# Performance work log

Measured on AMD Instinct MI355X. Metric: run time of the kernel, lower is better.

## Reference

```python
import jax, jax.numpy as jnp
import numpy as np

EPS = 1e-7  # keras.backend.epsilon()
B, U, F = 1024, 256, 31
D = 1 + U + F  # features dim after concat


def setup_inputs() -> dict:
    key = jax.random.key(0)
    ks = jax.random.split(key, 9)
    s = 1.0 / np.sqrt(D)
    return {
        "last_cell": jax.random.uniform(ks[0], (B, U), dtype=jnp.float32),
        "input_precipitation": jax.random.uniform(ks[1], (B,), dtype=jnp.float32),
        "input_other_features": jax.random.normal(ks[2], (B, F), dtype=jnp.float32),
        "W_i": jax.random.normal(ks[3], (D, U), dtype=jnp.float32) * s,
        "b_i": jnp.zeros((U,), dtype=jnp.float32),
        "W_r": jax.random.normal(ks[4], (D, U * U), dtype=jnp.float32) * s,
        "b_r": jnp.zeros((U * U,), dtype=jnp.float32),
        "W_o": jax.random.normal(ks[5], (D, U), dtype=jnp.float32) * s,
        "b_o": jnp.zeros((U,), dtype=jnp.float32),
    }


def reference(last_cell, input_precipitation, input_other_features,
              W_i, b_i, W_r, b_r, W_o, b_o):
    # L1-normalize last cell state (mass fractions)
    l1 = jnp.sum(jnp.abs(last_cell), axis=-1, keepdims=True) + EPS
    last_cell_hat = last_cell / l1
    p = input_precipitation[:, None]  # [B,1]
    features = jnp.concatenate([p, last_cell_hat, input_other_features], axis=-1)  # [B,D]

    # input gate: sigmoid then L1-normalized across units (mass-conserving split)
    ig = jax.nn.sigmoid(features @ W_i + b_i)
    ig = ig / jnp.sum(jnp.abs(ig), axis=-1, keepdims=True)

    # redistribution matrix: relu, reshape [B,U,U], L1-normalize each row
    R = jax.nn.relu(features @ W_r + b_r).reshape(-1, U, U)
    R = R / jnp.sum(jnp.abs(R), axis=-1, keepdims=True)

    # output gate: sigmoid
    og = jax.nn.sigmoid(features @ W_o + b_o)

    cell_in = ig * p                                   # [B,U]
    cell_sys = jnp.einsum('bu,buv->bv', last_cell, R)  # batched (1xU)@(UxU)
    candidate = cell_in + cell_sys
    output = og * candidate
    cell = (1.0 - og) * candidate
    return (cell, output)
```

## Files before the change

### kernel.cpp

```cpp
#include <hip/hip_runtime.h>


#define EPS_L1 1e-7f

constexpr int BB  = 1024;
constexpr int U   = 256;
constexpr int F   = 31;
constexpr int D   = 1 + U + F;
constexpr int NBV = BB * U;
constexpr int NCH = D / 32;
constexpr int UIMGB = NCH * 16384;
constexpr size_t WTB_BYTES  = (size_t)258 * UIMGB;
constexpr size_t FEAT_BYTES = (size_t)BB * D * 2;
constexpr int PITCH = 260;

typedef float f32x4 __attribute__((ext_vector_type(4)));
typedef short bf16x8 __attribute__((ext_vector_type(8)));

__device__ __forceinline__ unsigned f2bf(float x) {
  union { float f; unsigned u; } v; v.f = x;
  unsigned r = v.u + 0x7FFFu + ((v.u >> 16) & 1u);
  return r >> 16;
}

#define GLDS16(gp, lp)                                                        \
  __builtin_amdgcn_global_load_lds(                                          \
      (const __attribute__((address_space(1))) void*)(gp),                   \
      (__attribute__((address_space(3))) void*)(lp), 16, 0, 0)

#define MFMA16(a, b, c) __builtin_amdgcn_mfma_f32_16x16x32_bf16((a), (b), (c), 0, 0, 0)

__global__ __launch_bounds__(256) void k_prep(
    const float* __restrict__ lc, const float* __restrict__ p,
    const float* __restrict__ other,
    const float* __restrict__ Wi, const float* __restrict__ Wr,
    const float* __restrict__ Wo,
    short* __restrict__ WtB, short* __restrict__ featImg,
    float* __restrict__ cell_sys) {
  __shared__ short lds[2][32 * PITCH];
  __shared__ float inv_s[64];
  const int bid = blockIdx.x, t = threadIdx.x;

  if (bid < 774) {
    const int u = bid / 3, part = bid % 3;
    const float* src; long ld;
    if (u < 256)       { src = Wr + (size_t)u * 256; ld = 65536; }
    else if (u == 256) { src = Wi; ld = 256; }
    else               { src = Wo; ld = 256; }
    short* dst = WtB + (size_t)u * 73728;
    const int lane = t & 63, wave = t >> 6;
    const int g = lane >> 4, l15 = lane & 15;

#pragma unroll
    for (int cc = 0; cc < 3; ++cc) {
      const int c = part * 3 + cc;
      short* buf = lds[cc & 1];
#pragma unroll
      for (int i = 0; i < 8; ++i) {
        const int f = i * 256 + t;
        const int row = f >> 6, col4 = f & 63;
        const float4 v = *(const float4*)(src + (size_t)(c * 32 + row) * ld + col4 * 4);
        const unsigned lo = f2bf(v.x) | (f2bf(v.y) << 16);
        const unsigned hi = f2bf(v.z) | (f2bf(v.w) << 16);
        unsigned* wp = (unsigned*)&buf[row * PITCH + col4 * 4];
        wp[0] = lo; wp[1] = hi;
      }
      __syncthreads();
#pragma unroll
      for (int i = 0; i < 4; ++i) {
        const int n0 = wave * 4 + i;
        bf16x8 h;
#pragma unroll
        for (int j = 0; j < 8; ++j)
          h[j] = buf[(g * 8 + j) * PITCH + n0 * 16 + l15];
        *(bf16x8*)(dst + (size_t)(c * 16 + n0) * 512 + lane * 8) = h;
      }
      __syncthreads();
    }
  } else if (bid < 790) {
    const int mb = bid - 774;
    const int b0 = mb * 64;
    const int row = t >> 2, q = t & 3;
    const float4* lp = (const float4*)(lc + (size_t)(b0 + row) * 256 + q * 64);
    float s = 0.f;
#pragma unroll
    for (int j = 0; j < 16; ++j) {
      const float4 v = lp[j];
      s += fabsf(v.x) + fabsf(v.y) + fabsf(v.z) + fabsf(v.w);
    }
    s += __shfl_xor(s, 1, 64);
    s += __shfl_xor(s, 2, 64);
    if (q == 0) inv_s[row] = 1.f / (s + EPS_L1);
    __syncthreads();
#pragma unroll
    for (int i = 0; i < 9; ++i) {
      const int idx = i * 256 + t;
      const int reg = idx >> 6, l = idx & 63;
      const int c = reg >> 2, mt = reg & 3;
      const int lrow = mt * 16 + (l & 15);
      const int grow = b0 + lrow;
      const int k0 = c * 32 + (l >> 4) * 8;
      bf16x8 h;
#pragma unroll
      for (int j = 0; j < 8; ++j) {
        const int k = k0 + j;
        float v;
        if (k == 0) v = p[grow];
        else if (k <= 256) v = lc[(size_t)grow * 256 + (k - 1)] * inv_s[lrow];
        else v = other[(size_t)grow * 31 + (k - 257)];
        h[j] = (short)f2bf(v);
      }
      *(bf16x8*)(featImg + (size_t)mb * 18432 + (size_t)reg * 512 + l * 8) = h;
    }
  } else {
    float4* cs4 = (float4*)cell_sys;
    const int base = (bid - 790) * 8192 + t;
    const float4 z = {0.f, 0.f, 0.f, 0.f};
#pragma unroll
    for (int k2 = 0; k2 < 32; ++k2) cs4[base + k2 * 256] = z;
  }
}

__global__ __launch_bounds__(512, 2) void k_heavyR5(
    const short* __restrict__ featImg, const short* __restrict__ WtB,
    const float* __restrict__ lc, const float* __restrict__ br,
    float* __restrict__ cell_sys) {
  __shared__ short aT[36864];
  __shared__ float rsum[2][128][4];
  __shared__ float lcs[2][128];

  const int t = threadIdx.x, lane = t & 63, wave = t >> 6;
  const int cq = wave & 3, rh = wave >> 2;
  const int quad = lane >> 4, l15 = lane & 15;
  const int bid = blockIdx.x;
  const int Mb = bid >> 5, ug = bid & 31;
  const int b0 = Mb * 128, u0 = ug * 8;

  {
    const char* gA = (const char*)featImg + (size_t)Mb * 73728;
    char* lA = (char*)aT;
#pragma unroll
    for (int i = 0; i < 9; ++i)
      GLDS16(gA + i * 8192 + t * 16, lA + i * 8192 + t * 16);
  }

  const char* aB = (const char*)aT + rh * 36864 + lane * 16;
  const char* bB = (const char*)WtB + (size_t)u0 * UIMGB + cq * 4096 + lane * 16;

  f32x4 acc[4][4], outa[4][4];
#pragma unroll
  for (int m = 0; m < 4; ++m)
#pragma unroll
    for (int n = 0; n < 4; ++n)
#pragma unroll
      for (int r = 0; r < 4; ++r) { acc[m][n][r] = 0.f; outa[m][n][r] = 0.f; }

  bf16x8 bfr[3][4];
#pragma unroll
  for (int n = 0; n < 4; ++n) bfr[0][n] = *(const bf16x8*)(bB + n * 1024);
#pragma unroll
  for (int n = 0; n < 4; ++n) bfr[1][n] = *(const bf16x8*)(bB + 16384 + n * 1024);

  __syncthreads();

  bf16x8 afr[2][4];
#pragma unroll
  for (int m = 0; m < 4; ++m) afr[0][m] = *(const bf16x8*)(aB + m * 1024);

  for (int uu = 0; uu < 8; ++uu) {
    const int u = u0 + uu;
    float bv[4];

#pragma unroll
    for (int c = 0; c < 9; ++c) {
      if (c == 0) {
#pragma unroll
        for (int n = 0; n < 4; ++n)
          bv[n] = br[(size_t)u * 256 + cq * 64 + n * 16 + l15];
        if (t < 128) lcs[uu & 1][t] = lc[(size_t)(b0 + t) * 256 + u];
      }
#pragma unroll
      for (int n = 0; n < 4; ++n)
        bfr[(c + 2) % 3][n] = *(const bf16x8*)(bB + (c + 2) * 16384 + n * 1024);
      if (c < 8) {
#pragma unroll
        for (int m = 0; m < 4; ++m)
          afr[(c + 1) & 1][m] = *(const bf16x8*)(aB + (c + 1) * 4096 + m * 1024);
      }
#pragma unroll
      for (int m = 0; m < 4; ++m)
#pragma unroll
        for (int n = 0; n < 4; ++n)
          acc[m][n] = MFMA16(afr[c & 1][m], bfr[c % 3][n], acc[m][n]);
    }
    bB += UIMGB;

#pragma unroll
    for (int m = 0; m < 4; ++m) afr[0][m] = *(const bf16x8*)(aB + m * 1024);

    const int ub = uu & 1;
    float sm[4][4];
#pragma unroll
    for (int m = 0; m < 4; ++m)
#pragma unroll
      for (int r = 0; r < 4; ++r) {
        float sv = 0.f;
#pragma unroll
        for (int n = 0; n < 4; ++n) {
          const float rv = fmaxf(acc[m][n][r] + bv[n], 0.f);
          acc[m][n][r] = rv;
          sv += rv;
        }
        sm[m][r] = sv;
      }
#pragma unroll
    for (int msk = 1; msk < 16; msk <<= 1)
#pragma unroll
      for (int m = 0; m < 4; ++m)
#pragma unroll
        for (int r = 0; r < 4; ++r)
          sm[m][r] += __shfl_xor(sm[m][r], msk, 64);
    if (l15 == 0) {
#pragma unroll
      for (int m = 0; m < 4; ++m)
#pragma unroll
        for (int r = 0; r < 4; ++r)
          rsum[ub][rh * 64 + m * 16 + quad * 4 + r][cq] = sm[m][r];
    }
    __syncthreads();
#pragma unroll
    for (int m = 0; m < 4; ++m)
#pragma unroll
      for (int r = 0; r < 4; ++r) {
        const int row = rh * 64 + m * 16 + quad * 4 + r;
        const float4 rv = *(const float4*)&rsum[ub][row][0];
        const float tot = (rv.x + rv.y) + (rv.z + rv.w);
        const float alpha = lcs[ub][row] * __builtin_amdgcn_rcpf(tot);
#pragma unroll
        for (int n = 0; n < 4; ++n) {
          outa[m][n][r] = fmaf(alpha, acc[m][n][r], outa[m][n][r]);
          acc[m][n][r] = 0.f;
        }
      }
  }

#pragma unroll
  for (int m = 0; m < 4; ++m)
#pragma unroll
    for (int r = 0; r < 4; ++r) {
      const int grow = b0 + rh * 64 + m * 16 + quad * 4 + r;
#pragma unroll
      for (int n = 0; n < 4; ++n)
        atomicAdd(&cell_sys[(size_t)grow * 256 + cq * 64 + n * 16 + l15],
                  outa[m][n][r]);
    }
}

__global__ __launch_bounds__(512, 2) void k_post(
    const short* __restrict__ featImg, const short* __restrict__ WtB,
    const float* __restrict__ bi, const float* __restrict__ bo,
    const float* __restrict__ p, const float* __restrict__ cell_sys,
    float* __restrict__ dout) {
  __shared__ short aT[18432];
  __shared__ float rsum[64][12];
  __shared__ float ps[64];

  const int t = threadIdx.x, lane = t & 63, cg = t >> 6;
  const int quad = lane >> 4, l15 = lane & 15;
  const int mb = blockIdx.x, b0 = mb * 64;

  {
    const char* gsrc = (const char*)featImg + (size_t)mb * 36864;
    char* lbase = (char*)aT;
#pragma unroll
    for (int i = 0; i < 5; ++i) {
      if (i * 8 + cg < 36) {
        const int off = i * 8192 + t * 16;
        GLDS16(gsrc + off, lbase + off);
      }
    }
  }
  if (t < 64) ps[t] = p[b0 + t];

  f32x4 acc[4][2];
#pragma unroll
  for (int mt = 0; mt < 4; ++mt)
#pragma unroll
    for (int n = 0; n < 2; ++n)
#pragma unroll
      for (int r = 0; r < 4; ++r) acc[mt][n][r] = 0.f;

  const char* bptr = (const char*)WtB + (size_t)256 * UIMGB + cg * 2048 + lane * 16;
  bf16x8 cb0 = *(const bf16x8*)(bptr);
  bf16x8 cb1 = *(const bf16x8*)(bptr + 1024);
  bf16x8 nb0 = *(const bf16x8*)(bptr + 16384);
  bf16x8 nb1 = *(const bf16x8*)(bptr + 16384 + 1024);
  bptr += 32768;

  __syncthreads();

  float ig0[4][4], ig1[4][4], og0[4][4], og1[4][4];

#pragma unroll
  for (int g = 0; g < 2; ++g) {
    const float* bias = (g == 0) ? bi : bo;
    const float bv0 = bias[cg * 32 + l15];
    const float bv1 = bias[cg * 32 + 16 + l15];
#pragma unroll
    for (int c = 0; c < 9; ++c) {
      const bf16x8 pb0 = *(const bf16x8*)(bptr);
      const bf16x8 pb1 = *(const bf16x8*)(bptr + 1024);
      bptr += 16384;
      const char* ab = (const char*)aT + c * 4096 + lane * 16;
      const bf16x8 a0 = *(const bf16x8*)(ab);
      const bf16x8 a1 = *(const bf16x8*)(ab + 1024);
      const bf16x8 a2 = *(const bf16x8*)(ab + 2048);
      const bf16x8 a3 = *(const bf16x8*)(ab + 3072);
      acc[0][0] = MFMA16(a0, cb0, acc[0][0]);
      acc[0][1] = MFMA16(a0, cb1, acc[0][1]);
      acc[1][0] = MFMA16(a1, cb0, acc[1][0]);
      acc[1][1] = MFMA16(a1, cb1, acc[1][1]);
      acc[2][0] = MFMA16(a2, cb0, acc[2][0]);
      acc[2][1] = MFMA16(a2, cb1, acc[2][1]);
      acc[3][0] = MFMA16(a3, cb0, acc[3][0]);
      acc[3][1] = MFMA16(a3, cb1, acc[3][1]);
      cb0 = nb0; cb1 = nb1; nb0 = pb0; nb1 = pb1;
    }

#pragma unroll
    for (int mt = 0; mt < 4; ++mt)
#pragma unroll
      for (int r = 0; r < 4; ++r) {
        const float v0 = 1.f / (1.f + __expf(-(acc[mt][0][r] + bv0)));
        const float v1 = 1.f / (1.f + __expf(-(acc[mt][1][r] + bv1)));
        if (g == 0) { ig0[mt][r] = v0; ig1[mt][r] = v1; }
        else        { og0[mt][r] = v0; og1[mt][r] = v1; }
        acc[mt][0][r] = 0.f;
        acc[mt][1][r] = 0.f;
      }

    if (g == 0) {
      float sm[4][4];
#pragma unroll
      for (int mt = 0; mt < 4; ++mt)
#pragma unroll
        for (int r = 0; r < 4; ++r) sm[mt][r] = ig0[mt][r] + ig1[mt][r];
#pragma unroll
      for (int msk = 1; msk < 16; msk <<= 1)
#pragma unroll
        for (int mt = 0; mt < 4; ++mt)
#pragma unroll
          for (int r = 0; r < 4; ++r)
            sm[mt][r] += __shfl_xor(sm[mt][r], msk, 64);
      if (l15 == 0) {
#pragma unroll
        for (int mt = 0; mt < 4; ++mt)
#pragma unroll
          for (int r = 0; r < 4; ++r)
            rsum[mt * 16 + quad * 4 + r][cg] = sm[mt][r];
      }
      __syncthreads();
#pragma unroll
      for (int mt = 0; mt < 4; ++mt)
#pragma unroll
        for (int r = 0; r < 4; ++r) {
          const int row = mt * 16 + quad * 4 + r;
          const float4 ra = *(const float4*)&rsum[row][0];
          const float4 rb = *(const float4*)&rsum[row][4];
          const float inv = 1.f / (((ra.x + ra.y) + (ra.z + ra.w)) +
                                   ((rb.x + rb.y) + (rb.z + rb.w)));
          ig0[mt][r] *= inv;
          ig1[mt][r] *= inv;
        }
    }
  }

#pragma unroll
  for (int mt = 0; mt < 4; ++mt)
#pragma unroll
    for (int r = 0; r < 4; ++r) {
      const int row = mt * 16 + quad * 4 + r;
      const float pr = ps[row];
      const size_t base = (size_t)(b0 + row) * 256 + cg * 32 + l15;
      {
        const float cand = fmaf(ig0[mt][r], pr, cell_sys[base]);
        dout[base] = (1.f - og0[mt][r]) * cand;
        dout[NBV + base] = og0[mt][r] * cand;
      }
      {
        const float cand = fmaf(ig1[mt][r], pr, cell_sys[base + 16]);
        dout[base + 16] = (1.f - og1[mt][r]) * cand;
        dout[NBV + base + 16] = og1[mt][r] * cand;
      }
    }
}

extern "C" void kernel_launch(void* const* d_in, const int* in_sizes, int n_in,
                              void* d_out, int out_size, void* d_ws, size_t ws_size,
                              hipStream_t stream) {
  const float* lc    = (const float*)d_in[0];
  const float* p     = (const float*)d_in[1];
  const float* other = (const float*)d_in[2];
  const float* Wi    = (const float*)d_in[3];
  const float* bi    = (const float*)d_in[4];
  const float* Wr    = (const float*)d_in[5];
  const float* br    = (const float*)d_in[6];
  const float* Wo    = (const float*)d_in[7];
  const float* bo    = (const float*)d_in[8];
  float* out = (float*)d_out;

  char* wsb = (char*)d_ws;
  short* WtB      = (short*)wsb;
  short* featImg  = (short*)(wsb + WTB_BYTES);
  float* cell_sys = (float*)(wsb + WTB_BYTES + FEAT_BYTES);

  k_prep<<<798, 256, 0, stream>>>(lc, p, other, Wi, Wr, Wo, WtB, featImg, cell_sys);
  k_heavyR5<<<256, 512, 0, stream>>>(featImg, WtB, lc, br, cell_sys);
  k_post<<<16, 512, 0, stream>>>(featImg, WtB, bi, bo, p, cell_sys, out);
}
```

Baseline: 220.6 us.

## Halve heavy-kernel row tile to 64 and split prep into weight and feature kernels

```diff
diff --git a/kernel.cpp b/kernel.cpp
--- a/kernel.cpp
+++ b/kernel.cpp
@@ -30,56 +30,56 @@
 
 #define MFMA16(a, b, c) __builtin_amdgcn_mfma_f32_16x16x32_bf16((a), (b), (c), 0, 0, 0)
 
-__global__ __launch_bounds__(256) void k_prep(
+__global__ __launch_bounds__(256) void k_prepW(
+    const float* __restrict__ Wi, const float* __restrict__ Wr,
+    const float* __restrict__ Wo, short* __restrict__ WtB) {
+  __shared__ short lds[2][32 * PITCH];
+  const int bid = blockIdx.x, t = threadIdx.x;
+  const int u = bid / 3, part = bid % 3;
+  const float* src; long ld;
+  if (u < 256)       { src = Wr + (size_t)u * 256; ld = 65536; }
+  else if (u == 256) { src = Wi; ld = 256; }
+  else               { src = Wo; ld = 256; }
+  short* dst = WtB + (size_t)u * 73728;
+  const int lane = t & 63, wave = t >> 6;
+  const int g = lane >> 4, l15 = lane & 15;
+
+#pragma unroll
+  for (int cc = 0; cc < 3; ++cc) {
+    const int c = part * 3 + cc;
+    short* buf = lds[cc & 1];
+#pragma unroll
+    for (int i = 0; i < 8; ++i) {
+      const int f = i * 256 + t;
+      const int row = f >> 6, col4 = f & 63;
+      const float4 v = *(const float4*)(src + (size_t)(c * 32 + row) * ld + col4 * 4);
+      const unsigned lo = f2bf(v.x) | (f2bf(v.y) << 16);
+      const unsigned hi = f2bf(v.z) | (f2bf(v.w) << 16);
+      unsigned* wp = (unsigned*)&buf[row * PITCH + col4 * 4];
+      wp[0] = lo; wp[1] = hi;
+    }
+    __syncthreads();
+#pragma unroll
+    for (int i = 0; i < 4; ++i) {
+      const int n0 = wave * 4 + i;
+      bf16x8 h;
+#pragma unroll
+      for (int j = 0; j < 8; ++j)
+        h[j] = buf[(g * 8 + j) * PITCH + n0 * 16 + l15];
+      *(bf16x8*)(dst + (size_t)(c * 16 + n0) * 512 + lane * 8) = h;
+    }
+    __syncthreads();
+  }
+}
+
+__global__ __launch_bounds__(256) void k_prepF(
     const float* __restrict__ lc, const float* __restrict__ p,
-    const float* __restrict__ other,
-    const float* __restrict__ Wi, const float* __restrict__ Wr,
-    const float* __restrict__ Wo,
-    short* __restrict__ WtB, short* __restrict__ featImg,
+    const float* __restrict__ other, short* __restrict__ featImg,
     float* __restrict__ cell_sys) {
-  __shared__ short lds[2][32 * PITCH];
   __shared__ float inv_s[64];
   const int bid = blockIdx.x, t = threadIdx.x;
-
-  if (bid < 774) {
-    const int u = bid / 3, part = bid % 3;
-    const float* src; long ld;
-    if (u < 256)       { src = Wr + (size_t)u * 256; ld = 65536; }
-    else if (u == 256) { src = Wi; ld = 256; }
-    else               { src = Wo; ld = 256; }
-    short* dst = WtB + (size_t)u * 73728;
-    const int lane = t & 63, wave = t >> 6;
-    const int g = lane >> 4, l15 = lane & 15;
-
-#pragma unroll
-    for (int cc = 0; cc < 3; ++cc) {
-      const int c = part * 3 + cc;
-      short* buf = lds[cc & 1];
-#pragma unroll
-      for (int i = 0; i < 8; ++i) {
-        const int f = i * 256 + t;
-        const int row = f >> 6, col4 = f & 63;
-        const float4 v = *(const float4*)(src + (size_t)(c * 32 + row) * ld + col4 * 4);
-        const unsigned lo = f2bf(v.x) | (f2bf(v.y) << 16);
-        const unsigned hi = f2bf(v.z) | (f2bf(v.w) << 16);
-        unsigned* wp = (unsigned*)&buf[row * PITCH + col4 * 4];
-        wp[0] = lo; wp[1] = hi;
-      }
-      __syncthreads();
-#pragma unroll
-      for (int i = 0; i < 4; ++i) {
-        const int n0 = wave * 4 + i;
-        bf16x8 h;
-#pragma unroll
-        for (int j = 0; j < 8; ++j)
-          h[j] = buf[(g * 8 + j) * PITCH + n0 * 16 + l15];
-        *(bf16x8*)(dst + (size_t)(c * 16 + n0) * 512 + lane * 8) = h;
-      }
-      __syncthreads();
-    }
-  } else if (bid < 790) {
-    const int mb = bid - 774;
-    const int b0 = mb * 64;
+  if (bid < 16) {
+    const int b0 = bid * 64;
     const int row = t >> 2, q = t & 3;
     const float4* lp = (const float4*)(lc + (size_t)(b0 + row) * 256 + q * 64);
     float s = 0.f;
@@ -110,41 +110,41 @@
         else v = other[(size_t)grow * 31 + (k - 257)];
         h[j] = (short)f2bf(v);
       }
-      *(bf16x8*)(featImg + (size_t)mb * 18432 + (size_t)reg * 512 + l * 8) = h;
+      *(bf16x8*)(featImg + (size_t)bid * 18432 + (size_t)reg * 512 + l * 8) = h;
     }
   } else {
     float4* cs4 = (float4*)cell_sys;
-    const int base = (bid - 790) * 8192 + t;
+    const int base = (bid - 16) * 8192 + t;
     const float4 z = {0.f, 0.f, 0.f, 0.f};
 #pragma unroll
     for (int k2 = 0; k2 < 32; ++k2) cs4[base + k2 * 256] = z;
   }
 }
 
-__global__ __launch_bounds__(512, 2) void k_heavyR5(
+__global__ __launch_bounds__(256, 2) void k_heavyR6(
     const short* __restrict__ featImg, const short* __restrict__ WtB,
     const float* __restrict__ lc, const float* __restrict__ br,
     float* __restrict__ cell_sys) {
-  __shared__ short aT[36864];
-  __shared__ float rsum[2][128][4];
-  __shared__ float lcs[2][128];
-
-  const int t = threadIdx.x, lane = t & 63, wave = t >> 6;
-  const int cq = wave & 3, rh = wave >> 2;
+  __shared__ short aT[18432];
+  __shared__ float rsum[2][64][4];
+  __shared__ float lcs[2][64];
+
+  const int t = threadIdx.x, lane = t & 63, cq = t >> 6;
   const int quad = lane >> 4, l15 = lane & 15;
   const int bid = blockIdx.x;
-  const int Mb = bid >> 5, ug = bid & 31;
-  const int b0 = Mb * 128, u0 = ug * 8;
+  const int Mb = (bid >> 3) & 15;
+  const int ug = (bid & 7) * 4 + (bid >> 7);
+  const int b0 = Mb * 64, u0 = ug * 8;
 
   {
-    const char* gA = (const char*)featImg + (size_t)Mb * 73728;
+    const char* gA = (const char*)featImg + (size_t)Mb * 36864;
     char* lA = (char*)aT;
 #pragma unroll
     for (int i = 0; i < 9; ++i)
-      GLDS16(gA + i * 8192 + t * 16, lA + i * 8192 + t * 16);
-  }
-
-  const char* aB = (const char*)aT + rh * 36864 + lane * 16;
+      GLDS16(gA + i * 4096 + t * 16, lA + i * 4096 + t * 16);
+  }
+
+  const char* aB = (const char*)aT + lane * 16;
   const char* bB = (const char*)WtB + (size_t)u0 * UIMGB + cq * 4096 + lane * 16;
 
   f32x4 acc[4][4], outa[4][4];
@@ -170,15 +170,13 @@
   for (int uu = 0; uu < 8; ++uu) {
     const int u = u0 + uu;
     float bv[4];
+#pragma unroll
+    for (int n = 0; n < 4; ++n)
+      bv[n] = br[(size_t)u * 256 + cq * 64 + n * 16 + l15];
+    if (t < 64) lcs[uu & 1][t] = lc[(size_t)(b0 + t) * 256 + u];
 
 #pragma unroll
     for (int c = 0; c < 9; ++c) {
-      if (c == 0) {
-#pragma unroll
-        for (int n = 0; n < 4; ++n)
-          bv[n] = br[(size_t)u * 256 + cq * 64 + n * 16 + l15];
-        if (t < 128) lcs[uu & 1][t] = lc[(size_t)(b0 + t) * 256 + u];
-      }
 #pragma unroll
       for (int n = 0; n < 4; ++n)
         bfr[(c + 2) % 3][n] = *(const bf16x8*)(bB + (c + 2) * 16384 + n * 1024);
@@ -225,14 +223,14 @@
       for (int m = 0; m < 4; ++m)
 #pragma unroll
         for (int r = 0; r < 4; ++r)
-          rsum[ub][rh * 64 + m * 16 + quad * 4 + r][cq] = sm[m][r];
+          rsum[ub][m * 16 + quad * 4 + r][cq] = sm[m][r];
     }
     __syncthreads();
 #pragma unroll
     for (int m = 0; m < 4; ++m)
 #pragma unroll
       for (int r = 0; r < 4; ++r) {
-        const int row = rh * 64 + m * 16 + quad * 4 + r;
+        const int row = m * 16 + quad * 4 + r;
         const float4 rv = *(const float4*)&rsum[ub][row][0];
         const float tot = (rv.x + rv.y) + (rv.z + rv.w);
         const float alpha = lcs[ub][row] * __builtin_amdgcn_rcpf(tot);
@@ -248,7 +246,7 @@
   for (int m = 0; m < 4; ++m)
 #pragma unroll
     for (int r = 0; r < 4; ++r) {
-      const int grow = b0 + rh * 64 + m * 16 + quad * 4 + r;
+      const int grow = b0 + m * 16 + quad * 4 + r;
 #pragma unroll
       for (int n = 0; n < 4; ++n)
         atomicAdd(&cell_sys[(size_t)grow * 256 + cq * 64 + n * 16 + l15],
@@ -414,7 +412,8 @@
   short* featImg  = (short*)(wsb + WTB_BYTES);
   float* cell_sys = (float*)(wsb + WTB_BYTES + FEAT_BYTES);
 
-  k_prep<<<798, 256, 0, stream>>>(lc, p, other, Wi, Wr, Wo, WtB, featImg, cell_sys);
-  k_heavyR5<<<256, 512, 0, stream>>>(featImg, WtB, lc, br, cell_sys);
+  k_prepW<<<774, 256, 0, stream>>>(Wi, Wr, Wo, WtB);
+  k_prepF<<<24, 256, 0, stream>>>(lc, p, other, featImg, cell_sys);
+  k_heavyR6<<<512, 256, 0, stream>>>(featImg, WtB, lc, br, cell_sys);
   k_post<<<16, 512, 0, stream>>>(featImg, WtB, bi, bo, p, cell_sys, out);
 }
```

Measured after the change: 222.8 us. About the same (+1.0%).
